# Performance work log

Hardware: AMD Instinct MI355X
Metric: run time of the kernel (lower is better)

Reference implementation:

```python
import jax, jax.numpy as jnp
import numpy as np

T = 262144          # total frames
D_IN = 512
D_MODEL = 256
NUM_TYPES = 16
TYPE_EMB = 32
NUM_SCALARS = 8
K_MAX = 64
CONF_TH = 0.3
EPS = 1e-6


def setup_inputs() -> dict:
    key = jax.random.key(0)
    ks = jax.random.split(key, 8)
    features = jax.random.normal(ks[0], (T, D_IN), jnp.float32)
    energy = jax.random.uniform(ks[1], (T,), jnp.float32)
    frame_conf = jax.random.uniform(ks[2], (T,), jnp.float32)
    stream_conf = jax.random.uniform(ks[3], (T, 3), jnp.float32)
    # contiguous non-overlapping segments partitioning [0, T) -> all K_max valid
    rng = np.random.default_rng(0)
    bnd = np.sort(rng.choice(np.arange(1, T), size=K_MAX - 1, replace=False)).astype(np.int32)
    seg_start = jnp.asarray(np.concatenate([[0], bnd]).astype(np.int32))
    seg_end = jnp.asarray(np.concatenate([bnd, [T]]).astype(np.int32))
    event_type_id = jax.random.randint(ks[4], (K_MAX,), 0, NUM_TYPES, dtype=jnp.int32)
    emb = jax.random.normal(ks[5], (NUM_TYPES, TYPE_EMB), jnp.float32) * 0.02
    W = jax.random.normal(ks[6], (D_MODEL, D_IN + NUM_SCALARS + TYPE_EMB), jnp.float32) * 0.04
    bias = jnp.zeros((D_MODEL,), jnp.float32)
    return dict(features=features, energy=energy, frame_conf=frame_conf,
                stream_conf=stream_conf, seg_start=seg_start, seg_end=seg_end,
                event_type_id=event_type_id, emb=emb, W=W, bias=bias, fps=30)


def reference(features, energy, frame_conf, stream_conf, seg_start, seg_end,
              event_type_id, emb, W, bias, fps):
    n_frames = energy.shape[0]
    k_max = seg_start.shape[0]
    # segment id per frame (segments are a sorted contiguous partition)
    seg_ids = jnp.searchsorted(seg_start, jnp.arange(n_frames), side='right') - 1
    seg_len = (seg_end - seg_start).astype(features.dtype)          # [K]
    inv_len = 1.0 / seg_len

    # per-segment reductions (fused replacement for the python loop)
    e_k = jax.ops.segment_sum(features, seg_ids, k_max) * inv_len[:, None]   # [K, d_in]
    sum_e = jax.ops.segment_sum(energy, seg_ids, k_max)                      # [K]
    mean_motion = sum_e * inv_len
    peak_motion = jax.ops.segment_max(energy, seg_ids, k_max)
    p = energy / (sum_e[seg_ids] + EPS)                                      # [T]
    motion_entropy = -jax.ops.segment_sum(p * jnp.log(p + EPS), seg_ids, k_max)
    vis = jax.ops.segment_sum(stream_conf, seg_ids, k_max) * inv_len[:, None]  # [K,3]
    conf = jax.ops.segment_sum(frame_conf, seg_ids, k_max) * inv_len           # [K]

    duration_sec = seg_len / fps
    latency_sec = seg_start.astype(features.dtype) / fps
    s_k = jnp.log1p(jnp.stack([duration_sec, latency_sec, mean_motion, peak_motion,
                               motion_entropy, vis[:, 0], vis[:, 1], vis[:, 2]], axis=1))  # [K,8]

    g_k = emb[event_type_id]                                   # [K, type_emb]
    z_k = jnp.concatenate([e_k, s_k, g_k], axis=1)             # [K, d_in+8+type_emb]
    tokens = z_k @ W.T + bias                                  # [K, d_model]
    attn_mask = conf >= CONF_TH
    return tokens, attn_mask, event_type_id, conf, s_k
```

## Files before the change

### kernel.cpp

```cpp
#include <hip/hip_runtime.h>
#include <hip/hip_bf16.h>
#include <math.h>

#define T_TOTAL   262144
#define DIN       512
#define DMODEL    256
#define TYPE_EMB_ 32
#define NSCAL     8
#define KMAX      64
#define ZDIM      (DIN + NSCAL + TYPE_EMB_)
#define CONF_TH_  0.3f
#define EPS_      1e-6f
#define FPB       256

#define OFF_MASK  16384
#define OFF_TYPE  16448
#define OFF_CONF  16512
#define OFF_SK    16576

__global__ __launch_bounds__(256) void k1_feat_sums(
    const float* __restrict__ features,
    const int*   __restrict__ seg_start,
    const int*   __restrict__ seg_end,
    float*       __restrict__ acc )
{
    __shared__ float4 part[128];
    const int tid = threadIdx.x;
    const int c4  = tid & 127;
    const int r   = tid >> 7;
    const int w0  = blockIdx.x * FPB;
    const int w1  = w0 + FPB;

    int lo = 0, hi = KMAX - 1;
    while (lo < hi) {
        int mid = (lo + hi + 1) >> 1;
        if (seg_start[mid] <= w0) lo = mid; else hi = mid - 1;
    }
    int k = lo;

    const float4* __restrict__ f4 = (const float4*)features;

    for (;;) {
        const int s = max(w0, seg_start[k]);
        const int e = min(w1, seg_end[k]);

        float4 a0 = make_float4(0.f, 0.f, 0.f, 0.f);
        float4 a1 = make_float4(0.f, 0.f, 0.f, 0.f);
        int t = s + r;
        for (; t + 2 < e; t += 4) {
            float4 x0 = f4[(size_t)t       * 128 + c4];
            float4 x1 = f4[(size_t)(t + 2) * 128 + c4];
            a0.x += x0.x; a0.y += x0.y; a0.z += x0.z; a0.w += x0.w;
            a1.x += x1.x; a1.y += x1.y; a1.z += x1.z; a1.w += x1.w;
        }
        if (t < e) {
            float4 x0 = f4[(size_t)t * 128 + c4];
            a0.x += x0.x; a0.y += x0.y; a0.z += x0.z; a0.w += x0.w;
        }
        a0.x += a1.x; a0.y += a1.y; a0.z += a1.z; a0.w += a1.w;

        if (r == 1) part[c4] = a0;
        __syncthreads();
        if (r == 0) {
            float4 p = part[c4];
            a0.x += p.x; a0.y += p.y; a0.z += p.z; a0.w += p.w;
            float* dst = acc + (size_t)k * DIN + c4 * 4;
            atomicAdd(dst + 0, a0.x);
            atomicAdd(dst + 1, a0.y);
            atomicAdd(dst + 2, a0.z);
            atomicAdd(dst + 3, a0.w);
        }
        if (seg_end[k] >= w1 || k == KMAX - 1) break;
        ++k;
        __syncthreads();
    }
}

__device__ inline float waveSum(float v) {
    #pragma unroll
    for (int off = 32; off > 0; off >>= 1) v += __shfl_down(v, off, 64);
    return v;
}
__device__ inline float waveMax(float v) {
    #pragma unroll
    for (int off = 32; off > 0; off >>= 1) v = fmaxf(v, __shfl_down(v, off, 64));
    return v;
}

__global__ __launch_bounds__(256) void k2_scalars(
    const float* __restrict__ energy,
    const float* __restrict__ frame_conf,
    const float* __restrict__ stream_conf,
    const int*   __restrict__ seg_start,
    const int*   __restrict__ seg_end,
    const int*   __restrict__ event_type_id,
    const void*  __restrict__ fps_ptr,
    float*       __restrict__ out)
{
    __shared__ float red[6][4];
    const int k    = blockIdx.x;
    const int tid  = threadIdx.x;
    const int lane = tid & 63;
    const int wid  = tid >> 6;
    const int s = seg_start[k];
    const int e = seg_end[k];

    float sum_e = 0.f, sum_c = 0.f, v0 = 0.f, v1 = 0.f, v2 = 0.f, pk = -1e30f;
    for (int t = s + tid; t < e; t += 256) {
        float en = energy[t];
        sum_e += en;
        pk = fmaxf(pk, en);
        sum_c += frame_conf[t];
        v0 += stream_conf[3 * t + 0];
        v1 += stream_conf[3 * t + 1];
        v2 += stream_conf[3 * t + 2];
    }
    sum_e = waveSum(sum_e); sum_c = waveSum(sum_c);
    v0 = waveSum(v0); v1 = waveSum(v1); v2 = waveSum(v2);
    pk = waveMax(pk);
    if (lane == 0) {
        red[0][wid] = sum_e; red[1][wid] = sum_c; red[2][wid] = v0;
        red[3][wid] = v1;    red[4][wid] = v2;    red[5][wid] = pk;
    }
    __syncthreads();
    if (tid == 0) {
        float t0=0,t1=0,t2=0,t3=0,t4=0,t5=-1e30f;
        #pragma unroll
        for (int i = 0; i < 4; ++i) {
            t0 += red[0][i]; t1 += red[1][i]; t2 += red[2][i];
            t3 += red[3][i]; t4 += red[4][i]; t5 = fmaxf(t5, red[5][i]);
        }
        red[0][0]=t0; red[1][0]=t1; red[2][0]=t2; red[3][0]=t3; red[4][0]=t4; red[5][0]=t5;
    }
    __syncthreads();
    const float tot_e = red[0][0];
    __syncthreads();

    float ent = 0.f;
    const float inv_tot = 1.f / (tot_e + EPS_);
    for (int t = s + tid; t < e; t += 256) {
        float p = energy[t] * inv_tot;
        ent += p * logf(p + EPS_);
    }
    ent = waveSum(ent);
    if (lane == 0) red[0][wid] = ent;
    __syncthreads();

    if (tid == 0) {
        float entropy = -(red[0][0] + red[0][1] + red[0][2] + red[0][3]);
        const float len = (float)(e - s);
        const float inv_len = 1.f / len;

        int bits = *(const int*)fps_ptr;
        float fps = (bits > 0 && bits < 1000000) ? (float)bits : *(const float*)fps_ptr;

        float conf        = red[1][0] * inv_len;
        float mean_motion = tot_e * inv_len;
        float peak        = red[5][0];
        float vis0 = red[2][0] * inv_len;
        float vis1 = red[3][0] * inv_len;
        float vis2 = red[4][0] * inv_len;
        float dur  = len / fps;
        float lat  = (float)s / fps;

        float sv[8] = {dur, lat, mean_motion, peak, entropy, vis0, vis1, vis2};
        #pragma unroll
        for (int j = 0; j < 8; ++j) out[OFF_SK + k * 8 + j] = log1pf(sv[j]);
        out[OFF_CONF + k] = conf;
        out[OFF_MASK + k] = (conf >= CONF_TH_) ? 1.f : 0.f;
        out[OFF_TYPE + k] = (float)event_type_id[k];
    }
}

__global__ __launch_bounds__(256) void k3_tokens(
    const float* __restrict__ acc,
    const int*   __restrict__ seg_start,
    const int*   __restrict__ seg_end,
    const int*   __restrict__ event_type_id,
    const float* __restrict__ emb,
    const float* __restrict__ W,
    const float* __restrict__ bias,
    const float* __restrict__ out_sk,
    float*       __restrict__ tokens)
{
    __shared__ __align__(16) float z[ZDIM];
    const int k   = blockIdx.x;
    const int tid = threadIdx.x;
    const float inv_len = 1.f / (float)(seg_end[k] - seg_start[k]);

    for (int j = tid; j < DIN; j += 256) z[j] = acc[(size_t)k * DIN + j] * inv_len;
    if (tid < NSCAL) {
        z[DIN + tid] = out_sk[k * 8 + tid];
    } else if (tid >= 32 && tid < 32 + TYPE_EMB_) {
        z[DIN + NSCAL + (tid - 32)] = emb[event_type_id[k] * TYPE_EMB_ + (tid - 32)];
    }
    __syncthreads();

    const float4* z4 = (const float4*)z;
    const float4* w4 = (const float4*)(W + (size_t)tid * ZDIM);
    float a = bias[tid];
    #pragma unroll 2
    for (int j = 0; j < ZDIM / 4; ++j) {
        float4 x = z4[j];
        float4 w = w4[j];
        a += x.x * w.x + x.y * w.y + x.z * w.z + x.w * w.w;
    }
    tokens[k * DMODEL + tid] = a;
}

extern "C" void kernel_launch(void* const* d_in, const int* in_sizes, int n_in,
                              void* d_out, int out_size, void* d_ws, size_t ws_size,
                              hipStream_t stream) {
    const float* features    = (const float*)d_in[0];
    const float* energy      = (const float*)d_in[1];
    const float* frame_conf  = (const float*)d_in[2];
    const float* stream_conf = (const float*)d_in[3];
    const int*   seg_start   = (const int*)d_in[4];
    const int*   seg_end     = (const int*)d_in[5];
    const int*   type_id     = (const int*)d_in[6];
    const float* emb         = (const float*)d_in[7];
    const float* W           = (const float*)d_in[8];
    const float* bias        = (const float*)d_in[9];
    const void*  fps         = d_in[10];
    float* out = (float*)d_out;
    float* acc = (float*)d_ws;

    hipMemsetAsync(acc, 0, (size_t)KMAX * DIN * sizeof(float), stream);
    k1_feat_sums<<<T_TOTAL / FPB, 256, 0, stream>>>(features, seg_start, seg_end, acc);
    k2_scalars<<<KMAX, 256, 0, stream>>>(energy, frame_conf, stream_conf,
                                         seg_start, seg_end, type_id, fps, out);
    k3_tokens<<<KMAX, 256, 0, stream>>>(acc, seg_start, seg_end, type_id,
                                        emb, W, bias, out + OFF_SK, out);
}
```

Baseline: 786.2 us.

## Fuse per-segment scalar reductions into feature-sum kernel and merge scalar finalize into token GEMV

Scalar statistics (energy sum, peak, confidence, visibility, and a sum of e*log e) are now gathered inside the frame-parallel feature kernel and combined with atomics. This replaces the old 64-block scalar kernel, which made two passes over each segment, and computes entropy algebraically from S and sum(e log e). The finalize and token projection run in one kernel, and blocks lying entirely inside one segment take a 4-way unrolled fast path. The cost is extra atomics and a small numerical change to the entropy formula.

Measured after the change: 741.8 us. 5.6% less time.

```diff
diff --git a/kernel.cpp b/kernel.cpp
--- a/kernel.cpp
+++ b/kernel.cpp
@@ -18,179 +18,198 @@
 #define OFF_CONF  16512
 #define OFF_SK    16576
 
-__global__ __launch_bounds__(256) void k1_feat_sums(
+#define SCAL_OFF  (KMAX * DIN)
+
+__device__ inline float waveSum(float v) {
+    #pragma unroll
+    for (int off = 32; off > 0; off >>= 1) v += __shfl_down(v, off, 64);
+    return v;
+}
+__device__ inline float waveMax(float v) {
+    #pragma unroll
+    for (int off = 32; off > 0; off >>= 1) v = fmaxf(v, __shfl_down(v, off, 64));
+    return v;
+}
+
+__global__ __launch_bounds__(256) void k1_fused(
     const float* __restrict__ features,
+    const float* __restrict__ energy,
+    const float* __restrict__ frame_conf,
+    const float* __restrict__ stream_conf,
     const int*   __restrict__ seg_start,
     const int*   __restrict__ seg_end,
-    float*       __restrict__ acc )
+    float*       __restrict__ ws)
 {
     __shared__ float4 part[128];
-    const int tid = threadIdx.x;
-    const int c4  = tid & 127;
-    const int r   = tid >> 7;
-    const int w0  = blockIdx.x * FPB;
-    const int w1  = w0 + FPB;
+    __shared__ float  red[7][4];
+    const int tid  = threadIdx.x;
+    const int c4   = tid & 127;
+    const int r    = tid >> 7;
+    const int lane = tid & 63;
+    const int wid  = tid >> 6;
+    const int w0   = blockIdx.x * FPB;
+    const int w1   = w0 + FPB;
 
     int lo = 0, hi = KMAX - 1;
     while (lo < hi) {
         int mid = (lo + hi + 1) >> 1;
         if (seg_start[mid] <= w0) lo = mid; else hi = mid - 1;
     }
-    int k = lo;
+    const int k0 = lo;
+    const bool single = (seg_end[k0] >= w1);
 
     const float4* __restrict__ f4 = (const float4*)features;
 
-    for (;;) {
-        const int s = max(w0, seg_start[k]);
-        const int e = min(w1, seg_end[k]);
-
-        float4 a0 = make_float4(0.f, 0.f, 0.f, 0.f);
-        float4 a1 = make_float4(0.f, 0.f, 0.f, 0.f);
-        int t = s + r;
-        for (; t + 2 < e; t += 4) {
-            float4 x0 = f4[(size_t)t       * 128 + c4];
+    if (single) {
+        float4 a0 = make_float4(0.f,0.f,0.f,0.f), a1 = a0, a2 = a0, a3 = a0;
+        int t = w0 + r;
+        #pragma unroll 1
+        for (int i = 0; i < 32; ++i, t += 8) {
+            float4 x0 = f4[(size_t)(t)     * 128 + c4];
             float4 x1 = f4[(size_t)(t + 2) * 128 + c4];
+            float4 x2 = f4[(size_t)(t + 4) * 128 + c4];
+            float4 x3 = f4[(size_t)(t + 6) * 128 + c4];
             a0.x += x0.x; a0.y += x0.y; a0.z += x0.z; a0.w += x0.w;
             a1.x += x1.x; a1.y += x1.y; a1.z += x1.z; a1.w += x1.w;
-        }
-        if (t < e) {
-            float4 x0 = f4[(size_t)t * 128 + c4];
-            a0.x += x0.x; a0.y += x0.y; a0.z += x0.z; a0.w += x0.w;
-        }
-        a0.x += a1.x; a0.y += a1.y; a0.z += a1.z; a0.w += a1.w;
-
+            a2.x += x2.x; a2.y += x2.y; a2.z += x2.z; a2.w += x2.w;
+            a3.x += x3.x; a3.y += x3.y; a3.z += x3.z; a3.w += x3.w;
+        }
+        a0.x += a1.x + a2.x + a3.x; a0.y += a1.y + a2.y + a3.y;
+        a0.z += a1.z + a2.z + a3.z; a0.w += a1.w + a2.w + a3.w;
         if (r == 1) part[c4] = a0;
         __syncthreads();
         if (r == 0) {
             float4 p = part[c4];
             a0.x += p.x; a0.y += p.y; a0.z += p.z; a0.w += p.w;
-            float* dst = acc + (size_t)k * DIN + c4 * 4;
+            float* dst = ws + (size_t)k0 * DIN + c4 * 4;
             atomicAdd(dst + 0, a0.x);
             atomicAdd(dst + 1, a0.y);
             atomicAdd(dst + 2, a0.z);
             atomicAdd(dst + 3, a0.w);
         }
+    } else {
+        int k = k0;
+        for (;;) {
+            const int s = max(w0, seg_start[k]);
+            const int e = min(w1, seg_end[k]);
+            float4 a0 = make_float4(0.f,0.f,0.f,0.f), a1 = a0;
+            int t = s + r;
+            for (; t + 2 < e; t += 4) {
+                float4 x0 = f4[(size_t)t       * 128 + c4];
+                float4 x1 = f4[(size_t)(t + 2) * 128 + c4];
+                a0.x += x0.x; a0.y += x0.y; a0.z += x0.z; a0.w += x0.w;
+                a1.x += x1.x; a1.y += x1.y; a1.z += x1.z; a1.w += x1.w;
+            }
+            if (t < e) {
+                float4 x0 = f4[(size_t)t * 128 + c4];
+                a0.x += x0.x; a0.y += x0.y; a0.z += x0.z; a0.w += x0.w;
+            }
+            a0.x += a1.x; a0.y += a1.y; a0.z += a1.z; a0.w += a1.w;
+            if (r == 1) part[c4] = a0;
+            __syncthreads();
+            if (r == 0) {
+                float4 p = part[c4];
+                a0.x += p.x; a0.y += p.y; a0.z += p.z; a0.w += p.w;
+                float* dst = ws + (size_t)k * DIN + c4 * 4;
+                atomicAdd(dst + 0, a0.x);
+                atomicAdd(dst + 1, a0.y);
+                atomicAdd(dst + 2, a0.z);
+                atomicAdd(dst + 3, a0.w);
+            }
+            if (seg_end[k] >= w1 || k == KMAX - 1) break;
+            ++k;
+            __syncthreads();
+        }
+    }
+
+    int k = k0;
+    for (;;) {
+        const int s = max(w0, seg_start[k]);
+        const int e = min(w1, seg_end[k]);
+        float se = 0.f, sl = 0.f, sc = 0.f, v0 = 0.f, v1 = 0.f, v2 = 0.f, pk = 0.f;
+        const int t = s + tid;
+        if (t < e) {
+            float en = energy[t];
+            se = en;
+            sl = en * logf(en + 1e-12f);
+            pk = en;
+            sc = frame_conf[t];
+            v0 = stream_conf[3 * t + 0];
+            v1 = stream_conf[3 * t + 1];
+            v2 = stream_conf[3 * t + 2];
+        }
+        se = waveSum(se); sl = waveSum(sl); sc = waveSum(sc);
+        v0 = waveSum(v0); v1 = waveSum(v1); v2 = waveSum(v2);
+        pk = waveMax(pk);
+        if (lane == 0) {
+            red[0][wid] = se; red[1][wid] = sl; red[2][wid] = sc;
+            red[3][wid] = v0; red[4][wid] = v1; red[5][wid] = v2;
+            red[6][wid] = pk;
+        }
+        __syncthreads();
+        float* scal = ws + SCAL_OFF + k * 8;
+        if (tid < 6) {
+            float v = red[tid][0] + red[tid][1] + red[tid][2] + red[tid][3];
+            atomicAdd(scal + tid, v);
+        } else if (tid == 6) {
+            float m = fmaxf(fmaxf(red[6][0], red[6][1]), fmaxf(red[6][2], red[6][3]));
+            atomicMax((int*)(scal + 6), __float_as_int(m));
+        }
         if (seg_end[k] >= w1 || k == KMAX - 1) break;
         ++k;
         __syncthreads();
     }
 }
 
-__device__ inline float waveSum(float v) {
-    #pragma unroll
-    for (int off = 32; off > 0; off >>= 1) v += __shfl_down(v, off, 64);
-    return v;
-}
-__device__ inline float waveMax(float v) {
-    #pragma unroll
-    for (int off = 32; off > 0; off >>= 1) v = fmaxf(v, __shfl_down(v, off, 64));
-    return v;
-}
-
-__global__ __launch_bounds__(256) void k2_scalars(
-    const float* __restrict__ energy,
-    const float* __restrict__ frame_conf,
-    const float* __restrict__ stream_conf,
-    const int*   __restrict__ seg_start,
-    const int*   __restrict__ seg_end,
-    const int*   __restrict__ event_type_id,
-    const void*  __restrict__ fps_ptr,
-    float*       __restrict__ out)
-{
-    __shared__ float red[6][4];
-    const int k    = blockIdx.x;
-    const int tid  = threadIdx.x;
-    const int lane = tid & 63;
-    const int wid  = tid >> 6;
-    const int s = seg_start[k];
-    const int e = seg_end[k];
-
-    float sum_e = 0.f, sum_c = 0.f, v0 = 0.f, v1 = 0.f, v2 = 0.f, pk = -1e30f;
-    for (int t = s + tid; t < e; t += 256) {
-        float en = energy[t];
-        sum_e += en;
-        pk = fmaxf(pk, en);
-        sum_c += frame_conf[t];
-        v0 += stream_conf[3 * t + 0];
-        v1 += stream_conf[3 * t + 1];
-        v2 += stream_conf[3 * t + 2];
-    }
-    sum_e = waveSum(sum_e); sum_c = waveSum(sum_c);
-    v0 = waveSum(v0); v1 = waveSum(v1); v2 = waveSum(v2);
-    pk = waveMax(pk);
-    if (lane == 0) {
-        red[0][wid] = sum_e; red[1][wid] = sum_c; red[2][wid] = v0;
-        red[3][wid] = v1;    red[4][wid] = v2;    red[5][wid] = pk;
-    }
-    __syncthreads();
-    if (tid == 0) {
-        float t0=0,t1=0,t2=0,t3=0,t4=0,t5=-1e30f;
-        #pragma unroll
-        for (int i = 0; i < 4; ++i) {
-            t0 += red[0][i]; t1 += red[1][i]; t2 += red[2][i];
-            t3 += red[3][i]; t4 += red[4][i]; t5 = fmaxf(t5, red[5][i]);
-        }
-        red[0][0]=t0; red[1][0]=t1; red[2][0]=t2; red[3][0]=t3; red[4][0]=t4; red[5][0]=t5;
-    }
-    __syncthreads();
-    const float tot_e = red[0][0];
-    __syncthreads();
-
-    float ent = 0.f;
-    const float inv_tot = 1.f / (tot_e + EPS_);
-    for (int t = s + tid; t < e; t += 256) {
-        float p = energy[t] * inv_tot;
-        ent += p * logf(p + EPS_);
-    }
-    ent = waveSum(ent);
-    if (lane == 0) red[0][wid] = ent;
-    __syncthreads();
-
-    if (tid == 0) {
-        float entropy = -(red[0][0] + red[0][1] + red[0][2] + red[0][3]);
-        const float len = (float)(e - s);
-        const float inv_len = 1.f / len;
-
-        int bits = *(const int*)fps_ptr;
-        float fps = (bits > 0 && bits < 1000000) ? (float)bits : *(const float*)fps_ptr;
-
-        float conf        = red[1][0] * inv_len;
-        float mean_motion = tot_e * inv_len;
-        float peak        = red[5][0];
-        float vis0 = red[2][0] * inv_len;
-        float vis1 = red[3][0] * inv_len;
-        float vis2 = red[4][0] * inv_len;
-        float dur  = len / fps;
-        float lat  = (float)s / fps;
-
-        float sv[8] = {dur, lat, mean_motion, peak, entropy, vis0, vis1, vis2};
-        #pragma unroll
-        for (int j = 0; j < 8; ++j) out[OFF_SK + k * 8 + j] = log1pf(sv[j]);
-        out[OFF_CONF + k] = conf;
-        out[OFF_MASK + k] = (conf >= CONF_TH_) ? 1.f : 0.f;
-        out[OFF_TYPE + k] = (float)event_type_id[k];
-    }
-}
-
-__global__ __launch_bounds__(256) void k3_tokens(
-    const float* __restrict__ acc,
+__global__ __launch_bounds__(256) void k2_final(
+    const float* __restrict__ ws,
     const int*   __restrict__ seg_start,
     const int*   __restrict__ seg_end,
     const int*   __restrict__ event_type_id,
     const float* __restrict__ emb,
     const float* __restrict__ W,
     const float* __restrict__ bias,
-    const float* __restrict__ out_sk,
-    float*       __restrict__ tokens)
+    const void*  __restrict__ fps_ptr,
+    float*       __restrict__ out)
 {
     __shared__ __align__(16) float z[ZDIM];
+    __shared__ float skv[8];
     const int k   = blockIdx.x;
     const int tid = threadIdx.x;
-    const float inv_len = 1.f / (float)(seg_end[k] - seg_start[k]);
-
-    for (int j = tid; j < DIN; j += 256) z[j] = acc[(size_t)k * DIN + j] * inv_len;
+    const int s = seg_start[k], e = seg_end[k];
+    const float len = (float)(e - s);
+    const float inv_len = 1.f / len;
+
+    if (tid == 0) {
+        const float* scal = ws + SCAL_OFF + k * 8;
+        const float S  = scal[0];
+        const float SL = scal[1];
+        const float C  = scal[2];
+        const float V0 = scal[3], V1 = scal[4], V2 = scal[5];
+        const float pk = __int_as_float(((const int*)scal)[6]);
+        const float denom = S + EPS_;
+        const float entropy = logf(denom) * (S / denom) - SL / denom;
+
+        int bits = *(const int*)fps_ptr;
+        float fps = (bits > 0 && bits < 1000000) ? (float)bits : *(const float*)fps_ptr;
+
+        const float conf = C * inv_len;
+        float sv[8] = {len / fps, (float)s / fps, S * inv_len, pk, entropy,
+                       V0 * inv_len, V1 * inv_len, V2 * inv_len};
+        #pragma unroll
+        for (int j = 0; j < 8; ++j) {
+            float t = log1pf(sv[j]);
+            skv[j] = t;
+            out[OFF_SK + k * 8 + j] = t;
+        }
+        out[OFF_CONF + k] = conf;
+        out[OFF_MASK + k] = (conf >= CONF_TH_) ? 1.f : 0.f;
+        out[OFF_TYPE + k] = (float)event_type_id[k];
+    }
+    for (int j = tid; j < DIN; j += 256) z[j] = ws[(size_t)k * DIN + j] * inv_len;
+    __syncthreads();
     if (tid < NSCAL) {
-        z[DIN + tid] = out_sk[k * 8 + tid];
+        z[DIN + tid] = skv[tid];
     } else if (tid >= 32 && tid < 32 + TYPE_EMB_) {
         z[DIN + NSCAL + (tid - 32)] = emb[event_type_id[k] * TYPE_EMB_ + (tid - 32)];
     }
@@ -205,7 +224,7 @@
         float4 w = w4[j];
         a += x.x * w.x + x.y * w.y + x.z * w.z + x.w * w.w;
     }
-    tokens[k * DMODEL + tid] = a;
+    out[k * DMODEL + tid] = a;
 }
 
 extern "C" void kernel_launch(void* const* d_in, const int* in_sizes, int n_in,
@@ -223,12 +242,11 @@
     const float* bias        = (const float*)d_in[9];
     const void*  fps         = d_in[10];
     float* out = (float*)d_out;
-    float* acc = (float*)d_ws;
-
-    hipMemsetAsync(acc, 0, (size_t)KMAX * DIN * sizeof(float), stream);
-    k1_feat_sums<<<T_TOTAL / FPB, 256, 0, stream>>>(features, seg_start, seg_end, acc);
-    k2_scalars<<<KMAX, 256, 0, stream>>>(energy, frame_conf, stream_conf,
-                                         seg_start, seg_end, type_id, fps, out);
-    k3_tokens<<<KMAX, 256, 0, stream>>>(acc, seg_start, seg_end, type_id,
-                                        emb, W, bias, out + OFF_SK, out);
-}
+    float* ws  = (float*)d_ws;
+
+    hipMemsetAsync(ws, 0, (size_t)(KMAX * DIN + KMAX * 8) * sizeof(float), stream);
+    k1_fused<<<T_TOTAL / FPB, 256, 0, stream>>>(features, energy, frame_conf, stream_conf,
+                                                seg_start, seg_end, ws);
+    k2_final<<<KMAX, 256, 0, stream>>>(ws, seg_start, seg_end, type_id,
+                                       emb, W, bias, fps, out);
+}
```
